# Kernel tuning notes

Hardware: AMD Instinct MI355X
Metric: run time of the kernel (lower is better)

## Reference

```python
import jax, jax.numpy as jnp
import numpy as np

V, E, HL, HH, T_STEPS, N_STEPS = 32000, 768, 1024, 768, 5, 3
B, S = 8, 256
EPS = 1e-5


def _ln(x, g, b):
    m = jnp.mean(x, axis=-1, keepdims=True)
    v = jnp.var(x, axis=-1, keepdims=True)
    return (x - m) * jax.lax.rsqrt(v + EPS) * g + b


def _gru(x, h, Wi, bi, Wh, bh, lni_g, lni_b, lnh_g, lnh_b):
    # Wi: [3, in_dim, H]; gates stacked in order (r, z, n)
    xi = jnp.einsum('bd,kdh->kbh', x, Wi) + bi[:, None, :]
    hi = jnp.einsum('bh,khg->kbg', h, Wh) + bh[:, None, :]
    xi = _ln(xi, lni_g[:, None, :], lni_b[:, None, :])
    hi = _ln(hi, lnh_g[:, None, :], lnh_b[:, None, :])
    r = jax.nn.sigmoid(xi[0] + hi[0])
    z = jax.nn.sigmoid(xi[1] + hi[1])
    n = jnp.tanh(xi[2] + r * hi[2])
    return (1.0 - z) * n + z * h


def setup_inputs() -> dict:
    key = jax.random.key(0)
    ks = jax.random.split(key, 12)
    lin = E + HH  # low-level cell input dim (x concat h_h)

    def xavier(k, shape, fan_in, fan_out):
        lim = float(np.sqrt(6.0 / (fan_in + fan_out)))
        return jax.random.uniform(k, shape, jnp.float32, -lim, lim)

    inp = {
        'input_ids': jax.random.randint(ks[0], (B, S), 0, V),
        'emb': xavier(ks[1], (V, E), V, E),
        'ln_emb_g': jnp.ones((E,), jnp.float32),
        'ln_emb_b': jnp.zeros((E,), jnp.float32),
        'low_Wi': xavier(ks[2], (3, lin, HL), lin, HL),
        'low_bi': jnp.zeros((3, HL), jnp.float32),
        'low_Wh': xavier(ks[3], (3, HL, HL), HL, HL),
        'low_bh': jnp.zeros((3, HL), jnp.float32),
        'low_lni_g': jnp.ones((3, HL), jnp.float32),
        'low_lni_b': jnp.zeros((3, HL), jnp.float32),
        'low_lnh_g': jnp.ones((3, HL), jnp.float32),
        'low_lnh_b': jnp.zeros((3, HL), jnp.float32),
        'high_Wi': xavier(ks[4], (3, HL, HH), HL, HH),
        'high_bi': jnp.zeros((3, HH), jnp.float32),
        'high_Wh': xavier(ks[5], (3, HH, HH), HH, HH),
        'high_bh': jnp.zeros((3, HH), jnp.float32),
        'high_lni_g': jnp.ones((3, HH), jnp.float32),
        'high_lni_b': jnp.zeros((3, HH), jnp.float32),
        'high_lnh_g': jnp.ones((3, HH), jnp.float32),
        'high_lnh_b': jnp.zeros((3, HH), jnp.float32),
        'Wout': xavier(ks[6], (HH, V), HH, V),
        'bout': jnp.zeros((V,), jnp.float32),
    }
    return inp


def reference(input_ids, emb, ln_emb_g, ln_emb_b,
              low_Wi, low_bi, low_Wh, low_bh,
              low_lni_g, low_lni_b, low_lnh_g, low_lnh_b,
              high_Wi, high_bi, high_Wh, high_bh,
              high_lni_g, high_lni_b, high_lnh_g, high_lnh_b,
              Wout, bout):
    b = input_ids.shape[0]
    h_l0 = jnp.zeros((b, HL), jnp.float32)
    h_h0 = jnp.zeros((b, HH), jnp.float32)

    def step(carry, ids_t):
        h_l, h_h = carry
        x = _ln(emb[ids_t], ln_emb_g, ln_emb_b)  # [B, E]
        for _ in range(N_STEPS):
            for _ in range(T_STEPS):
                h_l = _gru(jnp.concatenate([x, h_h], axis=-1), h_l,
                           low_Wi, low_bi, low_Wh, low_bh,
                           low_lni_g, low_lni_b, low_lnh_g, low_lnh_b)
            h_h = _gru(h_l, h_h,
                       high_Wi, high_bi, high_Wh, high_bh,
                       high_lni_g, high_lni_b, high_lnh_g, high_lnh_b)
        logits_t = h_h @ Wout + bout  # [B, V]
        return (h_l, h_h), logits_t

    _, logits = jax.lax.scan(step, (h_l0, h_h0), input_ids.T)  # [S, B, V]
    return jnp.transpose(logits, (1, 0, 2))  # [B, S, V]
```

## Files before the change

### kernel.cpp

```cpp
#include <hip/hip_runtime.h>
#include <hip/hip_bf16.h>


#define NWG 128
#define NTH 256
#define EPSV 1e-5f
#define NROUND 4608

typedef __attribute__((ext_vector_type(4))) float f32x4;
typedef __attribute__((ext_vector_type(8))) short short8;
typedef unsigned long long u64;

struct PArgs {
  const int* ids; const float* emb; const float* lng; const float* lnb;
  const float* lWi; const float* lbi; const float* lWh; const float* lbh;
  const float* llig; const float* llib; const float* llhg; const float* llhb;
  const float* hWi; const float* hbi; const float* hWh; const float* hbh;
  const float* hlig; const float* hlib; const float* hlhg; const float* hlhb;
  int* arr; int* rel; int* cnt; u64* sredG; u64* statsG; float* hlR; float* hhR;
  __hip_bfloat16* hist; float* WiT; float* hWiT; float* hWhT;
};

__device__ __forceinline__ float sigm(float x) { return 1.f / (1.f + __expf(-x)); }
__device__ __forceinline__ float tanh_f(float x) {
  x = fminf(15.f, fmaxf(-15.f, x));
  float e = __expf(2.f * x);
  return (e - 1.f) / (e + 1.f);
}
__device__ __forceinline__ int aldi(const int* p) {
  return __hip_atomic_load(p, __ATOMIC_RELAXED, __HIP_MEMORY_SCOPE_AGENT);
}
__device__ __forceinline__ u64 aldu(const u64* p) {
  return __hip_atomic_load(p, __ATOMIC_RELAXED, __HIP_MEMORY_SCOPE_AGENT);
}
__device__ __forceinline__ void asti(int* p, int v) {
  __hip_atomic_store(p, v, __ATOMIC_RELAXED, __HIP_MEMORY_SCOPE_AGENT);
}
__device__ __forceinline__ u64 pk2(float a, float b) {
  union { u64 u; float f[2]; } c; c.f[0] = a; c.f[1] = b; return c.u;
}
__device__ __forceinline__ void astu(u64* p, u64 v) {
  __hip_atomic_store(p, v, __ATOMIC_RELAXED, __HIP_MEMORY_SCOPE_AGENT);
}
__device__ __forceinline__ void ast(float* p, float v) {
  __hip_atomic_store(p, v, __ATOMIC_RELAXED, __HIP_MEMORY_SCOPE_AGENT);
}
__device__ __forceinline__ void ald4x8(const float* p0, const float* p1,
                                       const float* p2, const float* p3,
                                       const float* p4, const float* p5,
                                       const float* p6, const float* p7,
                                       float4& a, float4& b, float4& c, float4& d,
                                       float4& e, float4& f, float4& g, float4& h) {
  asm volatile(
      "global_load_dwordx4 %0, %8, off sc1\n\t"
      "global_load_dwordx4 %1, %9, off sc1\n\t"
      "global_load_dwordx4 %2, %10, off sc1\n\t"
      "global_load_dwordx4 %3, %11, off sc1\n\t"
      "global_load_dwordx4 %4, %12, off sc1\n\t"
      "global_load_dwordx4 %5, %13, off sc1\n\t"
      "global_load_dwordx4 %6, %14, off sc1\n\t"
      "global_load_dwordx4 %7, %15, off sc1\n\t"
      "s_waitcnt vmcnt(0)"
      : "=&v"(a), "=&v"(b), "=&v"(c), "=&v"(d),
        "=&v"(e), "=&v"(f), "=&v"(g), "=&v"(h)
      : "v"(p0), "v"(p1), "v"(p2), "v"(p3),
        "v"(p4), "v"(p5), "v"(p6), "v"(p7)
      : "memory");
}
__device__ __forceinline__ void ald4x4(const float* p0, const float* p1,
                                       const float* p2, const float* p3,
                                       float4& a, float4& b, float4& c, float4& d) {
  asm volatile(
      "global_load_dwordx4 %0, %4, off sc1\n\t"
      "global_load_dwordx4 %1, %5, off sc1\n\t"
      "global_load_dwordx4 %2, %6, off sc1\n\t"
      "global_load_dwordx4 %3, %7, off sc1\n\t"
      "s_waitcnt vmcnt(0)"
      : "=&v"(a), "=&v"(b), "=&v"(c), "=&v"(d)
      : "v"(p0), "v"(p1), "v"(p2), "v"(p3)
      : "memory");
}
__device__ __forceinline__ void ald4x3(const float* p0, const float* p1,
                                       const float* p2,
                                       float4& a, float4& b, float4& c) {
  asm volatile(
      "global_load_dwordx4 %0, %3, off sc1\n\t"
      "global_load_dwordx4 %1, %4, off sc1\n\t"
      "global_load_dwordx4 %2, %5, off sc1\n\t"
      "s_waitcnt vmcnt(0)"
      : "=&v"(a), "=&v"(b), "=&v"(c)
      : "v"(p0), "v"(p1), "v"(p2)
      : "memory");
}

__global__ void __launch_bounds__(NTH) hrm_recur(PArgs P) {
  __shared__ float WhS[24 * 1024];
  __shared__ float Bb[8 * 1024];
  __shared__ float XW[24 * 8];
  __shared__ float xiNs[24 * 8];
  __shared__ float stg[2 * 24 * 8];
  __shared__ float sred[96];
  __shared__ float xm[8], xrs[8];
  __shared__ float mbuf[96][4];
  __shared__ int idsh[8];
  __shared__ int okf;

  const int tid = threadIdx.x;

  if (blockIdx.x >= NWG) {
    const int pl = blockIdx.x - NWG;
    #pragma unroll 1
    for (int r = 1; r <= NROUND; ++r) {
      if (tid < 64) {
        const u64* ap = (const u64*)(P.arr + pl * 128) + tid;
        int lim = 1 << 22, g1 = 1;
        for (;;) {
          u64 v = aldu(ap);
          int a0 = (int)(unsigned)(v & 0xffffffffull);
          int a1 = (int)(unsigned)(v >> 32);
          if (__all(a0 >= r && a1 >= r)) break;
          if (--lim == 0) { g1 = 0; break; }
          __builtin_amdgcn_s_sleep(1);
        }
        if (tid == 0) okf = g1;
      }
      __syncthreads();
      if (!okf) {
        if (tid < 8) asti(P.rel + pl * 128 + tid * 16, 1 << 30);
        return;
      }
      const int ph = (r - 1) % 6;
      const bool full = (ph == 0 || ph == 5);
      const int lo = pl * 24 + (full ? 0 : 12);
      const int n  = full ? 24 : 12;
      const float invD = (ph == 5) ? (1.f / 768.f) : (1.f / 1024.f);
      const int par = r & 1;
      if (tid < (n >> 1) * 8) {
        int rp = (lo >> 1) + (tid >> 3), q = tid & 7;
        const float* fb = (const float*)(P.statsG + (size_t)par * 128 * 48);
        float4 s; s.x = 0.f; s.y = 0.f; s.z = 0.f; s.w = 0.f;
        #pragma unroll
        for (int blk = 0; blk < 2; ++blk) {
          int w0 = q * 16 + blk * 8;
          float4 t0,t1,t2,t3,t4,t5,t6,t7;
          ald4x8(fb + (size_t)(w0+0)*96 + rp*4, fb + (size_t)(w0+1)*96 + rp*4,
                 fb + (size_t)(w0+2)*96 + rp*4, fb + (size_t)(w0+3)*96 + rp*4,
                 fb + (size_t)(w0+4)*96 + rp*4, fb + (size_t)(w0+5)*96 + rp*4,
                 fb + (size_t)(w0+6)*96 + rp*4, fb + (size_t)(w0+7)*96 + rp*4,
                 t0,t1,t2,t3,t4,t5,t6,t7);
          s.x += t0.x+t1.x+t2.x+t3.x+t4.x+t5.x+t6.x+t7.x;
          s.y += t0.y+t1.y+t2.y+t3.y+t4.y+t5.y+t6.y+t7.y;
          s.z += t0.z+t1.z+t2.z+t3.z+t4.z+t5.z+t6.z+t7.z;
          s.w += t0.w+t1.w+t2.w+t3.w+t4.w+t5.w+t6.w+t7.w;
        }
        mbuf[tid][0] = s.x; mbuf[tid][1] = s.y; mbuf[tid][2] = s.z; mbuf[tid][3] = s.w;
      }
      __syncthreads();
      if (tid < n) {
        int rpl = tid >> 1, comp = tid & 1;
        float s1 = 0.f, s2 = 0.f;
        #pragma unroll
        for (int q = 0; q < 8; ++q) {
          s1 += mbuf[rpl * 8 + q][comp * 2 + 0];
          s2 += mbuf[rpl * 8 + q][comp * 2 + 1];
        }
        float m = s1 * invD;
        float rs = rsqrtf(s2 * invD - m * m + EPSV);
        astu(P.sredG + (size_t)pl * 96 + (size_t)par * 48 + lo + tid, pk2(m, rs));
      }
      asm volatile("s_waitcnt vmcnt(0)" ::: "memory");
      __syncthreads();
      if (tid < 8) asti(P.rel + pl * 128 + tid * 16, r);
    }
    return;
  }

  const int wg = blockIdx.x;
  const int ks = tid & 31, cg = tid >> 5;
  const int lj8 = wg * 8, lj6 = wg * 6;
  const int rep = wg & 3;

  auto arriveA = [&](int pl, int r) {
    asm volatile("s_waitcnt vmcnt(0)" ::: "memory");
    __syncthreads();
    if (tid == 0) asti(P.arr + pl * 128 + wg, r);
  };
  auto pollRel = [&](int pl, int r, bool full) -> bool {
    if (tid == 0) {
      const int* rp = P.rel + pl * 128 + (wg & 7) * 16;
      int lim = 1 << 22, v = 0;
      do {
        v = aldi(rp);
        if (v >= r) break;
        __builtin_amdgcn_s_sleep(1);
      } while (--lim);
      okf = (lim != 0 && v < (1 << 29)) ? 1 : 0;
    }
    __syncthreads();
    if (okf) {
      int lo = pl * 24 + (full ? 0 : 12);
      int n  = full ? 24 : 12;
      if (tid < n) {
        int row = lo + tid;
        union { u64 u; float f[2]; } c;
        c.u = aldu(P.sredG + (size_t)pl * 96 + (size_t)(r & 1) * 48 + row);
        int local = row - pl * 24;
        int set = local / 12, rem = local % 12, g = rem >> 2, bq = rem & 3;
        int b = pl * 4 + bq;
        sred[set * 48 + g * 16 + b * 2] = c.f[0];
        sred[set * 48 + g * 16 + b * 2 + 1] = c.f[1];
      }
      __syncthreads();
    }
    return okf != 0;
  };
  auto waitB = [&](int pl, int target) -> bool {
    if (tid < 64) {
      bool active = tid < 8;
      const int* cp = P.cnt + pl * 256 + (size_t)(active ? tid : 0) * 32;
      int lim = 1 << 22;
      for (;;) {
        int v = active ? aldi(cp) : 0;
        int sum = v;
        sum += __shfl_xor(sum, 1);
        sum += __shfl_xor(sum, 2);
        sum += __shfl_xor(sum, 4);
        int total = __shfl(sum, 0);
        if (total >= target) break;
        if (--lim == 0) break;
        __builtin_amdgcn_s_sleep(2);
      }
      if (tid == 0) okf = (lim != 0) ? 1 : 0;
    }
    __syncthreads();
    return okf != 0;
  };
  auto gate_commit = [&](int pl) {
    asm volatile("s_waitcnt vmcnt(0)" ::: "memory");
    if (tid == 0)
      __hip_atomic_fetch_add(P.cnt + pl * 256 + (size_t)(wg & 7) * 32, 1,
                             __ATOMIC_RELAXED, __HIP_MEMORY_SCOPE_AGENT);
  };

  auto stage_hl = [&](int pl) {
    const float* base = P.hlR + (size_t)rep * 8192 + (size_t)pl * 4096 + tid * 4;
    float4 t0,t1,t2,t3;
    ald4x4(base + 0*1024, base + 1*1024, base + 2*1024, base + 3*1024,
           t0,t1,t2,t3);
    float* db = &Bb[pl * 4096 + tid * 4];
    *(float4*)&db[0*1024] = t0; *(float4*)&db[1*1024] = t1;
    *(float4*)&db[2*1024] = t2; *(float4*)&db[3*1024] = t3;
  };
  auto stage_hh = [&](int pl) {
    const float* base = P.hhR + (size_t)rep * 6144 + (size_t)pl * 3072;
    int bi[3], ki[3];
    #pragma unroll
    for (int i = 0; i < 3; ++i) {
      int c = i * 256 + tid; int bq = c / 192; int k = (c - bq * 192) * 4;
      bi[i] = bq; ki[i] = k;
    }
    float4 t0,t1,t2;
    ald4x3(base + bi[0]*768 + ki[0], base + bi[1]*768 + ki[1],
           base + bi[2]*768 + ki[2], t0,t1,t2);
    *(float4*)&Bb[(pl*4+bi[0])*1024 + ki[0]] = t0;
    *(float4*)&Bb[(pl*4+bi[1])*1024 + ki[1]] = t1;
    *(float4*)&Bb[(pl*4+bi[2])*1024 + ki[2]] = t2;
  };

  auto gemm_lowh = [&](int pl, float (&acc)[3][4]) {
    const int c0 = cg * 3;
    const float* w0p = &WhS[(c0 + 0) * 1024];
    const float* w1p = &WhS[(c0 + 1) * 1024];
    const float* w2p = &WhS[(c0 + 2) * 1024];
    const float* hb = &Bb[pl * 4096];
    #pragma unroll
    for (int i = 0; i < 8; ++i) {
      int k = i * 128 + ks * 4;
      float4 w0 = *(const float4*)&w0p[k];
      float4 w1 = *(const float4*)&w1p[k];
      float4 w2 = *(const float4*)&w2p[k];
      #pragma unroll
      for (int bq = 0; bq < 4; ++bq) {
        float4 h = *(const float4*)&hb[bq * 1024 + k];
        acc[0][bq] += w0.x*h.x + w0.y*h.y + w0.z*h.z + w0.w*h.w;
        acc[1][bq] += w1.x*h.x + w1.y*h.y + w1.z*h.z + w1.w*h.w;
        acc[2][bq] += w2.x*h.x + w2.y*h.y + w2.z*h.z + w2.w*h.w;
      }
    }
  };
  auto gemm_xih = [&](int pl, float (&acc)[3][4]) {
    const float* wp[3];
    #pragma unroll
    for (int cc = 0; cc < 3; ++cc) {
      int c = cg * 3 + cc; int g = c >> 3, jj = c & 7;
      wp[cc] = P.WiT + ((size_t)g * 1024 + lj8 + jj) * 1536 + 768;
    }
    const float* hb = &Bb[pl * 4096];
    #pragma unroll
    for (int i = 0; i < 6; ++i) {
      int k = i * 128 + ks * 4;
      float4 w0 = *(const float4*)&wp[0][k];
      float4 w1 = *(const float4*)&wp[1][k];
      float4 w2 = *(const float4*)&wp[2][k];
      #pragma unroll
      for (int bq = 0; bq < 4; ++bq) {
        float4 h = *(const float4*)&hb[bq * 1024 + k];
        acc[0][bq] += w0.x*h.x + w0.y*h.y + w0.z*h.z + w0.w*h.w;
        acc[1][bq] += w1.x*h.x + w1.y*h.y + w1.z*h.z + w1.w*h.w;
        acc[2][bq] += w2.x*h.x + w2.y*h.y + w2.z*h.z + w2.w*h.w;
      }
    }
  };
  auto gemm_hxi = [&](int pl, float (&acc)[3][4]) {
    if (cg >= 6) return;
    const float* wp[3];
    #pragma unroll
    for (int cc = 0; cc < 3; ++cc) {
      int c = cg * 3 + cc; int g = c / 6, jj = c % 6;
      wp[cc] = P.hWiT + ((size_t)g * 768 + lj6 + jj) * 1024;
    }
    const float* hb = &Bb[pl * 4096];
    #pragma unroll
    for (int i = 0; i < 8; ++i) {
      int k = i * 128 + ks * 4;
      float4 w0 = *(const float4*)&wp[0][k];
      float4 w1 = *(const float4*)&wp[1][k];
      float4 w2 = *(const float4*)&wp[2][k];
      #pragma unroll
      for (int bq = 0; bq < 4; ++bq) {
        float4 h = *(const float4*)&hb[bq * 1024 + k];
        acc[0][bq] += w0.x*h.x + w0.y*h.y + w0.z*h.z + w0.w*h.w;
        acc[1][bq] += w1.x*h.x + w1.y*h.y + w1.z*h.z + w1.w*h.w;
        acc[2][bq] += w2.x*h.x + w2.y*h.y + w2.z*h.z + w2.w*h.w;
      }
    }
  };
  auto gemm_hhh = [&](int pl, float (&acc)[3][4]) {
    if (cg >= 6) return;
    const float* wp[3];
    #pragma unroll
    for (int cc = 0; cc < 3; ++cc) {
      int c = cg * 3 + cc; int g = c / 6, jj = c % 6;
      wp[cc] = P.hWhT + ((size_t)g * 768 + lj6 + jj) * 768;
    }
    const float* hb = &Bb[pl * 4096];
    #pragma unroll
    for (int i = 0; i < 6; ++i) {
      int k = i * 128 + ks * 4;
      float4 w0 = *(const float4*)&wp[0][k];
      float4 w1 = *(const float4*)&wp[1][k];
      float4 w2 = *(const float4*)&wp[2][k];
      #pragma unroll
      for (int bq = 0; bq < 4; ++bq) {
        float4 h = *(const float4*)&hb[bq * 1024 + k];
        acc[0][bq] += w0.x*h.x + w0.y*h.y + w0.z*h.z + w0.w*h.w;
        acc[1][bq] += w1.x*h.x + w1.y*h.y + w1.z*h.z + w1.w*h.w;
        acc[2][bq] += w2.x*h.x + w2.y*h.y + w2.z*h.z + w2.w*h.w;
      }
    }
  };

  auto redstage = [&](int pl, float (&acc)[3][4], int set, const float* bias,
                      int dim, int perg, int jb, bool addXW) {
    #pragma unroll
    for (int cc = 0; cc < 3; ++cc)
      #pragma unroll
      for (int bq = 0; bq < 4; ++bq) {
        float v = acc[cc][bq];
        #pragma unroll
        for (int m = 1; m < 32; m <<= 1) v += __shfl_xor(v, m, 64);
        acc[cc][bq] = v;
      }
    if ((tid & 31) == 0) {
      int cgl = tid >> 5;
      #pragma unroll
      for (int cc = 0; cc < 3; ++cc) {
        int c = cgl * 3 + cc;
        if (c < perg * 3) {
          int g = (perg == 8) ? (c >> 3) : (c / 6);
          int jj = (perg == 8) ? (c & 7) : (c % 6);
          float bs = bias[g * dim + jb + jj];
          #pragma unroll
          for (int bq = 0; bq < 4; ++bq) {
            float v = acc[cc][bq] + bs;
            if (addXW) v += XW[c * 8 + pl * 4 + bq];
            stg[set * 192 + c * 8 + pl * 4 + bq] = v;
          }
        }
      }
    }
  };

  auto stats_put = [&](int pl, int par, int set, int perg) {
    if (tid < 12) {
      int g = tid >> 2, bq = tid & 3;
      float s1 = 0.f, s2 = 0.f;
      for (int jj = 0; jj < perg; ++jj) {
        float v = stg[set * 192 + (g * perg + jj) * 8 + pl * 4 + bq];
        s1 += v; s2 += v * v;
      }
      int row = pl * 24 + set * 12 + g * 4 + bq;
      astu(P.statsG + ((size_t)par * 128 + wg) * 48 + row, pk2(s1, s2));
    }
  };

  auto gate_low = [&](int pl, bool isA) {
    if (tid < 32) {
      int jj = tid & 7, bq = tid >> 3; int b = pl * 4 + bq; int j = lj8 + jj;
      float xin[3], hin[3];
      #pragma unroll
      for (int g = 0; g < 3; ++g) {
        int c = g * 8 + jj;
        if (isA) {
          float m = sred[g * 16 + b * 2], rs = sred[g * 16 + b * 2 + 1];
          float v = (stg[c * 8 + b] - m) * rs * P.llig[g * 1024 + j] + P.llib[g * 1024 + j];
          xiNs[c * 8 + b] = v; xin[g] = v;
        } else {
          xin[g] = xiNs[c * 8 + b];
        }
        float m2 = sred[48 + g * 16 + b * 2], rs2 = sred[48 + g * 16 + b * 2 + 1];
        hin[g] = (stg[192 + c * 8 + b] - m2) * rs2 * P.llhg[g * 1024 + j] + P.llhb[g * 1024 + j];
      }
      float rg = sigm(xin[0] + hin[0]);
      float zg = sigm(xin[1] + hin[1]);
      float ng = tanh_f(xin[2] + rg * hin[2]);
      float hold = Bb[b * 1024 + j];
      float hv = (1.f - zg) * ng + zg * hold;
      #pragma unroll
      for (int rp = 0; rp < 4; ++rp) ast(&P.hlR[rp * 8192 + b * 1024 + j], hv);
    }
  };

  auto gate_high = [&](int pl, int t, int nn) {
    if (tid < 24) {
      int jj = tid % 6, bq = tid / 6; int b = pl * 4 + bq; int j = lj6 + jj;
      float xin[3], hin[3];
      #pragma unroll
      for (int g = 0; g < 3; ++g) {
        int c = g * 6 + jj;
        float m = sred[g * 16 + b * 2], rs = sred[g * 16 + b * 2 + 1];
        xin[g] = (stg[c * 8 + b] - m) * rs * P.hlig[g * 768 + j] + P.hlib[g * 768 + j];
        float m2 = sred[48 + g * 16 + b * 2], rs2 = sred[48 + g * 16 + b * 2 + 1];
        hin[g] = (stg[192 + c * 8 + b] - m2) * rs2 * P.hlhg[g * 768 + j] + P.hlhb[g * 768 + j];
      }
      float rg = sigm(xin[0] + hin[0]);
      float zg = sigm(xin[1] + hin[1]);
      float ng = tanh_f(xin[2] + rg * hin[2]);
      float hold = Bb[b * 1024 + j];
      float hv = (1.f - zg) * ng + zg * hold;
      #pragma unroll
      for (int rp = 0; rp < 4; ++rp) ast(&P.hhR[rp * 6144 + b * 768 + j], hv);
      if (nn == 2) P.hist[((size_t)t * 8 + b) * 768 + j] = __float2bfloat16(hv);
    }
  };

  auto xfun = [&](int tt) {
    int bq = tid >> 5, u = tid & 31;
    if (tid < 8) idsh[tid] = P.ids[tid * 256 + tt];
    int id = P.ids[bq * 256 + tt];
    const float* e = P.emb + (size_t)id * 768;
    float s1 = 0.f, s2 = 0.f;
    #pragma unroll
    for (int q = 0; q < 24; q += 4) {
      float4 v = *(const float4*)&e[u * 24 + q];
      s1 += v.x + v.y + v.z + v.w;
      s2 += v.x*v.x + v.y*v.y + v.z*v.z + v.w*v.w;
    }
    #pragma unroll
    for (int m = 1; m < 32; m <<= 1) { s1 += __shfl_xor(s1, m, 64); s2 += __shfl_xor(s2, m, 64); }
    if (u == 0) { float mm = s1 / 768.f; xm[bq] = mm; xrs[bq] = rsqrtf(s2 / 768.f - mm * mm + EPSV); }
    __syncthreads();
    float acc[3][8] = {};
    const float* wp[3];
    #pragma unroll
    for (int cc = 0; cc < 3; ++cc) {
      int c = cg * 3 + cc; int g = c >> 3, jj = c & 7;
      wp[cc] = P.WiT + ((size_t)g * 1024 + lj8 + jj) * 1536;
    }
    int idv[8];
    #pragma unroll
    for (int bb = 0; bb < 8; ++bb) idv[bb] = idsh[bb];
// ... 57 lines not shown
      float vv[6] = {a.x, a.y, b2v.x, b2v.y, c2v.x, c2v.y};
      for (int jj = 0; jj < 6; ++jj)
        P.hWiT[((size_t)g * 768 + lj6 + jj) * 1024 + k] = vv[jj];
    }
  #pragma unroll 1
  for (int g = 0; g < 3; ++g)
    for (int it = 0; it < 3; ++it) {
      int k = it * 256 + tid;
      const float* src = P.hWh + ((size_t)g * 768 + k) * 768 + lj6;
      float2 a = *(const float2*)src, b2v = *(const float2*)(src + 2), c2v = *(const float2*)(src + 4);
      float vv[6] = {a.x, a.y, b2v.x, b2v.y, c2v.x, c2v.y};
      for (int jj = 0; jj < 6; ++jj)
        P.hWhT[((size_t)g * 768 + lj6 + jj) * 768 + k] = vv[jj];
    }
  #pragma unroll 1
  for (int g = 0; g < 3; ++g)
    for (int it = 0; it < 4; ++it) {
      int k = it * 256 + tid;
      const float* src = P.lWh + ((size_t)g * 1024 + k) * 1024 + lj8;
      float4 v0 = *(const float4*)src; float4 v1 = *(const float4*)(src + 4);
      float vv[8] = {v0.x, v0.y, v0.z, v0.w, v1.x, v1.y, v1.z, v1.w};
      for (int jj = 0; jj < 8; ++jj) WhS[(g * 8 + jj) * 1024 + k] = vv[jj];
    }
  __syncthreads();
  xfun(0);

  int r = 1;
  bool alive = true;
  #pragma unroll 1
  for (int t = 0; t < 256 && alive; ++t) {
    #pragma unroll 1
    for (int nn = 0; nn < 3 && alive; ++nn) {
      {
        #pragma unroll 1
        for (int pl = 0; pl < 2; ++pl) {
          alive = waitB(pl, NWG * (r - 1)); if (!alive) break;
          stage_hh(pl); __syncthreads();
          float aX[3][4] = {};
          gemm_xih(pl, aX);
          redstage(pl, aX, 0, P.lbi, 1024, 8, lj8, true);
          __syncthreads();
          stage_hl(pl); __syncthreads();
          float aH[3][4] = {};
          gemm_lowh(pl, aH);
          redstage(pl, aH, 1, P.lbh, 1024, 8, lj8, false);
          __syncthreads();
          stats_put(pl, r & 1, 0, 8); stats_put(pl, r & 1, 1, 8);
          arriveA(pl, r);
        }
        if (!alive) break;
        #pragma unroll 1
        for (int pl = 0; pl < 2; ++pl) {
          alive = pollRel(pl, r, true); if (!alive) break;
          gate_low(pl, true);
          gate_commit(pl);
        }
        if (!alive) break;
        ++r;
      }
      #pragma unroll 1
      for (int it = 1; it < 5 && alive; ++it) {
        #pragma unroll 1
        for (int pl = 0; pl < 2; ++pl) {
          alive = waitB(pl, NWG * (r - 1)); if (!alive) break;
          stage_hl(pl); __syncthreads();
          float a2[3][4] = {};
          gemm_lowh(pl, a2);
          redstage(pl, a2, 1, P.lbh, 1024, 8, lj8, false);
          __syncthreads();
          stats_put(pl, r & 1, 1, 8);
          arriveA(pl, r);
        }
        if (!alive) break;
        #pragma unroll 1
        for (int pl = 0; pl < 2; ++pl) {
          alive = pollRel(pl, r, false); if (!alive) break;
          gate_low(pl, false);
          gate_commit(pl);
        }
        if (!alive) break;
        ++r;
      }
      if (!alive) break;
      {
        #pragma unroll 1
        for (int pl = 0; pl < 2; ++pl) {
          alive = waitB(pl, NWG * (r - 1)); if (!alive) break;
          stage_hl(pl); __syncthreads();
          float aX[3][4] = {};
          gemm_hxi(pl, aX);
          redstage(pl, aX, 0, P.hbi, 768, 6, lj6, false);
          __syncthreads();
          stage_hh(pl); __syncthreads();
          float aH[3][4] = {};
          gemm_hhh(pl, aH);
          redstage(pl, aH, 1, P.hbh, 768, 6, lj6, false);
          __syncthreads();
          stats_put(pl, r & 1, 0, 6); stats_put(pl, r & 1, 1, 6);
          arriveA(pl, r);
        }
        if (!alive) break;
        #pragma unroll 1
        for (int pl = 0; pl < 2; ++pl) {
          alive = pollRel(pl, r, true); if (!alive) break;
          gate_high(pl, t, nn);
          gate_commit(pl);
        }
        if (!alive) break;
        ++r;
        if (nn == 2 && t < 255) { __syncthreads(); xfun(t + 1); }
      }
    }
  }
}

__global__ void __launch_bounds__(256) wout_t(const float* __restrict__ W,
                                              __hip_bfloat16* __restrict__ WT) {
  __shared__ float T[64][65];
  int n0 = blockIdx.x * 64, k0 = blockIdx.y * 64;
  int tid = threadIdx.x;
  int lane16 = tid & 15, grp = tid >> 4;
  #pragma unroll
  for (int i = 0; i < 4; ++i) {
    int kl = i * 16 + grp; int nl = lane16 * 4;
    float4 v = *(const float4*)&W[(size_t)(k0 + kl) * 32000 + n0 + nl];
    T[kl][nl] = v.x; T[kl][nl + 1] = v.y; T[kl][nl + 2] = v.z; T[kl][nl + 3] = v.w;
  }
  __syncthreads();
  #pragma unroll
  for (int i = 0; i < 4; ++i) {
    int nl = i * 16 + grp; int kl = lane16 * 4;
    union { ushort4 v; __hip_bfloat16 h[4]; } u;
    for (int q = 0; q < 4; ++q) u.h[q] = __float2bfloat16(T[kl + q][nl]);
    *(ushort4*)&WT[(size_t)(n0 + nl) * 768 + k0 + kl] = u.v;
  }
}

// ... 35 lines not shown
      for (int j = 0; j < 4; ++j)
        bfr[j] = *(short8*)&Bs[(wc * 64 + j * 16 + r16) * 64 + kk + khalf];
      #pragma unroll
      for (int i = 0; i < 4; ++i)
        #pragma unroll
        for (int j = 0; j < 4; ++j)
          acc[i][j] = __builtin_amdgcn_mfma_f32_16x16x32_bf16(af[i], bfr[j], acc[i][j], 0, 0, 0);
    }
  }
  #pragma unroll
  for (int i = 0; i < 4; ++i)
    #pragma unroll
    for (int j = 0; j < 4; ++j)
      #pragma unroll
      for (int q = 0; q < 4; ++q) {
        int m = m0 + wr * 64 + i * 16 + ((lane >> 4) * 4 + q);
        int n = n0 + wc * 64 + j * 16 + (lane & 15);
        out[(size_t)(m & 7) * 8192000 + (size_t)(m >> 3) * 32000 + n] =
            acc[i][j][q] + bias[n];
      }
}

extern "C" void kernel_launch(void* const* d_in, const int* in_sizes, int n_in,
                              void* d_out, int out_size, void* d_ws, size_t ws_size,
                              hipStream_t stream) {
  (void)in_sizes; (void)n_in; (void)out_size; (void)ws_size;
  char* wsb = (char*)d_ws;
  size_t off = 0;
  auto take = [&](size_t bytes) -> void* {
    void* p = wsb + off;
    off += (bytes + 1023) & ~(size_t)1023;
    return p;
  };
  int* arr    = (int*)take((size_t)2 * 128 * 4);
  int* rel    = (int*)take((size_t)2 * 128 * 4);
  int* cnt    = (int*)take((size_t)2 * 8 * 32 * 4);
  u64* sredG  = (u64*)take((size_t)2 * 2 * 48 * 8);
  float* hlR  = (float*)take((size_t)4 * 8 * 1024 * 4);
  float* hhR  = (float*)take((size_t)4 * 8 * 768 * 4);
  size_t state_bytes = off;
  u64* statsG = (u64*)take((size_t)2 * 128 * 48 * 8);
  __hip_bfloat16* hist = (__hip_bfloat16*)take((size_t)2048 * 768 * 2);
  float* WiT  = (float*)take((size_t)3 * 1024 * 1536 * 4);
  float* hWiT = (float*)take((size_t)3 * 768 * 1024 * 4);
  float* hWhT = (float*)take((size_t)3 * 768 * 768 * 4);
  __hip_bfloat16* WoutT = (__hip_bfloat16*)take((size_t)32000 * 768 * 2);

  hipMemsetAsync(d_ws, 0, state_bytes, stream);

  wout_t<<<dim3(500, 12), 256, 0, stream>>>((const float*)d_in[20], WoutT);

  PArgs A;
  A.ids = (const int*)d_in[0];   A.emb = (const float*)d_in[1];
  A.lng = (const float*)d_in[2]; A.lnb = (const float*)d_in[3];
  A.lWi = (const float*)d_in[4]; A.lbi = (const float*)d_in[5];
  A.lWh = (const float*)d_in[6]; A.lbh = (const float*)d_in[7];
  A.llig = (const float*)d_in[8];  A.llib = (const float*)d_in[9];
  A.llhg = (const float*)d_in[10]; A.llhb = (const float*)d_in[11];
  A.hWi = (const float*)d_in[12];  A.hbi = (const float*)d_in[13];
  A.hWh = (const float*)d_in[14];  A.hbh = (const float*)d_in[15];
  A.hlig = (const float*)d_in[16]; A.hlib = (const float*)d_in[17];
  A.hlhg = (const float*)d_in[18]; A.hlhb = (const float*)d_in[19];
  A.arr = arr; A.rel = rel; A.cnt = cnt; A.sredG = sredG; A.statsG = statsG;
  A.hlR = hlR; A.hhR = hhR;
  A.hist = hist; A.WiT = WiT; A.hWiT = hWiT; A.hWhT = hWhT;

  hrm_recur<<<NWG + 2, NTH, 0, stream>>>(A);

  logits_gemm<<<dim3(250, 16), 256, 0, stream>>>(hist, WoutT,
                                                 (const float*)d_in[21],
                                                 (float*)d_out);
}
```

Before: 59.90 ms.

## Replace dedicated stats-reducer blocks with atomic accumulation and counter polling

Removes the two extra reducer workgroups that gathered per-WG LayerNorm partial sums and released workers via arrive/release flags. Each worker now atomically adds its partial sums into 8 striped accumulators and bumps a striped counter. Every worker then polls the counter and finalizes the mean and rstd itself, double-buffering and zeroing the accumulators by parity. The aim is to cut one global synchronisation hop per phase, at the cost of float atomic contention and every WG redoing the small finalization.

```diff
diff --git a/kernel.cpp b/kernel.cpp
--- a/kernel.cpp
+++ b/kernel.cpp
@@ -5,7 +5,6 @@
 #define NWG 128
 #define NTH 256
 #define EPSV 1e-5f
-#define NROUND 4608
 
 typedef __attribute__((ext_vector_type(4))) float f32x4;
 typedef __attribute__((ext_vector_type(8))) short short8;
@@ -17,7 +16,7 @@
   const float* llig; const float* llib; const float* llhg; const float* llhb;
   const float* hWi; const float* hbi; const float* hWh; const float* hbh;
   const float* hlig; const float* hlib; const float* hlhg; const float* hlhb;
-  int* arr; int* rel; int* cnt; u64* sredG; u64* statsG; float* hlR; float* hhR;
+  int* cnt; int* scnt; float* statsA; float* hlR; float* hhR;
   __hip_bfloat16* hist; float* WiT; float* hWiT; float* hWhT;
 };
 
@@ -30,42 +29,11 @@
 __device__ __forceinline__ int aldi(const int* p) {
   return __hip_atomic_load(p, __ATOMIC_RELAXED, __HIP_MEMORY_SCOPE_AGENT);
 }
-__device__ __forceinline__ u64 aldu(const u64* p) {
-  return __hip_atomic_load(p, __ATOMIC_RELAXED, __HIP_MEMORY_SCOPE_AGENT);
-}
-__device__ __forceinline__ void asti(int* p, int v) {
-  __hip_atomic_store(p, v, __ATOMIC_RELAXED, __HIP_MEMORY_SCOPE_AGENT);
-}
-__device__ __forceinline__ u64 pk2(float a, float b) {
-  union { u64 u; float f[2]; } c; c.f[0] = a; c.f[1] = b; return c.u;
-}
 __device__ __forceinline__ void astu(u64* p, u64 v) {
   __hip_atomic_store(p, v, __ATOMIC_RELAXED, __HIP_MEMORY_SCOPE_AGENT);
 }
 __device__ __forceinline__ void ast(float* p, float v) {
   __hip_atomic_store(p, v, __ATOMIC_RELAXED, __HIP_MEMORY_SCOPE_AGENT);
-}
-__device__ __forceinline__ void ald4x8(const float* p0, const float* p1,
-                                       const float* p2, const float* p3,
-                                       const float* p4, const float* p5,
-                                       const float* p6, const float* p7,
-                                       float4& a, float4& b, float4& c, float4& d,
-                                       float4& e, float4& f, float4& g, float4& h) {
-  asm volatile(
-      "global_load_dwordx4 %0, %8, off sc1\n\t"
-      "global_load_dwordx4 %1, %9, off sc1\n\t"
-      "global_load_dwordx4 %2, %10, off sc1\n\t"
-      "global_load_dwordx4 %3, %11, off sc1\n\t"
-      "global_load_dwordx4 %4, %12, off sc1\n\t"
-      "global_load_dwordx4 %5, %13, off sc1\n\t"
-      "global_load_dwordx4 %6, %14, off sc1\n\t"
-      "global_load_dwordx4 %7, %15, off sc1\n\t"
-      "s_waitcnt vmcnt(0)"
-      : "=&v"(a), "=&v"(b), "=&v"(c), "=&v"(d),
-        "=&v"(e), "=&v"(f), "=&v"(g), "=&v"(h)
-      : "v"(p0), "v"(p1), "v"(p2), "v"(p3),
-        "v"(p4), "v"(p5), "v"(p6), "v"(p7)
-      : "memory");
 }
 __device__ __forceinline__ void ald4x4(const float* p0, const float* p1,
                                        const float* p2, const float* p3,
@@ -101,119 +69,15 @@
   __shared__ float stg[2 * 24 * 8];
   __shared__ float sred[96];
   __shared__ float xm[8], xrs[8];
-  __shared__ float mbuf[96][4];
   __shared__ int idsh[8];
   __shared__ int okf;
 
   const int tid = threadIdx.x;
-
-  if (blockIdx.x >= NWG) {
-    const int pl = blockIdx.x - NWG;
-    #pragma unroll 1
-    for (int r = 1; r <= NROUND; ++r) {
-      if (tid < 64) {
-        const u64* ap = (const u64*)(P.arr + pl * 128) + tid;
-        int lim = 1 << 22, g1 = 1;
-        for (;;) {
-          u64 v = aldu(ap);
-          int a0 = (int)(unsigned)(v & 0xffffffffull);
-          int a1 = (int)(unsigned)(v >> 32);
-          if (__all(a0 >= r && a1 >= r)) break;
-          if (--lim == 0) { g1 = 0; break; }
-          __builtin_amdgcn_s_sleep(1);
-        }
-        if (tid == 0) okf = g1;
-      }
-      __syncthreads();
-      if (!okf) {
-        if (tid < 8) asti(P.rel + pl * 128 + tid * 16, 1 << 30);
-        return;
-      }
-      const int ph = (r - 1) % 6;
-      const bool full = (ph == 0 || ph == 5);
-      const int lo = pl * 24 + (full ? 0 : 12);
-      const int n  = full ? 24 : 12;
-      const float invD = (ph == 5) ? (1.f / 768.f) : (1.f / 1024.f);
-      const int par = r & 1;
-      if (tid < (n >> 1) * 8) {
-        int rp = (lo >> 1) + (tid >> 3), q = tid & 7;
-        const float* fb = (const float*)(P.statsG + (size_t)par * 128 * 48);
-        float4 s; s.x = 0.f; s.y = 0.f; s.z = 0.f; s.w = 0.f;
-        #pragma unroll
-        for (int blk = 0; blk < 2; ++blk) {
-          int w0 = q * 16 + blk * 8;
-          float4 t0,t1,t2,t3,t4,t5,t6,t7;
-          ald4x8(fb + (size_t)(w0+0)*96 + rp*4, fb + (size_t)(w0+1)*96 + rp*4,
-                 fb + (size_t)(w0+2)*96 + rp*4, fb + (size_t)(w0+3)*96 + rp*4,
-                 fb + (size_t)(w0+4)*96 + rp*4, fb + (size_t)(w0+5)*96 + rp*4,
-                 fb + (size_t)(w0+6)*96 + rp*4, fb + (size_t)(w0+7)*96 + rp*4,
-                 t0,t1,t2,t3,t4,t5,t6,t7);
-          s.x += t0.x+t1.x+t2.x+t3.x+t4.x+t5.x+t6.x+t7.x;
-          s.y += t0.y+t1.y+t2.y+t3.y+t4.y+t5.y+t6.y+t7.y;
-          s.z += t0.z+t1.z+t2.z+t3.z+t4.z+t5.z+t6.z+t7.z;
-          s.w += t0.w+t1.w+t2.w+t3.w+t4.w+t5.w+t6.w+t7.w;
-        }
-        mbuf[tid][0] = s.x; mbuf[tid][1] = s.y; mbuf[tid][2] = s.z; mbuf[tid][3] = s.w;
-      }
-      __syncthreads();
-      if (tid < n) {
-        int rpl = tid >> 1, comp = tid & 1;
-        float s1 = 0.f, s2 = 0.f;
-        #pragma unroll
-        for (int q = 0; q < 8; ++q) {
-          s1 += mbuf[rpl * 8 + q][comp * 2 + 0];
-          s2 += mbuf[rpl * 8 + q][comp * 2 + 1];
-        }
-        float m = s1 * invD;
-        float rs = rsqrtf(s2 * invD - m * m + EPSV);
-        astu(P.sredG + (size_t)pl * 96 + (size_t)par * 48 + lo + tid, pk2(m, rs));
-      }
-      asm volatile("s_waitcnt vmcnt(0)" ::: "memory");
-      __syncthreads();
-      if (tid < 8) asti(P.rel + pl * 128 + tid * 16, r);
-    }
-    return;
-  }
-
   const int wg = blockIdx.x;
   const int ks = tid & 31, cg = tid >> 5;
   const int lj8 = wg * 8, lj6 = wg * 6;
   const int rep = wg & 3;
 
-  auto arriveA = [&](int pl, int r) {
-    asm volatile("s_waitcnt vmcnt(0)" ::: "memory");
-    __syncthreads();
-    if (tid == 0) asti(P.arr + pl * 128 + wg, r);
-  };
-  auto pollRel = [&](int pl, int r, bool full) -> bool {
-    if (tid == 0) {
-      const int* rp = P.rel + pl * 128 + (wg & 7) * 16;
-      int lim = 1 << 22, v = 0;
-      do {
-        v = aldi(rp);
-        if (v >= r) break;
-        __builtin_amdgcn_s_sleep(1);
-      } while (--lim);
-      okf = (lim != 0 && v < (1 << 29)) ? 1 : 0;
-    }
-    __syncthreads();
-    if (okf) {
-      int lo = pl * 24 + (full ? 0 : 12);
-      int n  = full ? 24 : 12;
-      if (tid < n) {
-        int row = lo + tid;
-        union { u64 u; float f[2]; } c;
-        c.u = aldu(P.sredG + (size_t)pl * 96 + (size_t)(r & 1) * 48 + row);
-        int local = row - pl * 24;
-        int set = local / 12, rem = local % 12, g = rem >> 2, bq = rem & 3;
-        int b = pl * 4 + bq;
-        sred[set * 48 + g * 16 + b * 2] = c.f[0];
-        sred[set * 48 + g * 16 + b * 2 + 1] = c.f[1];
-      }
-      __syncthreads();
-    }
-    return okf != 0;
-  };
   auto waitB = [&](int pl, int target) -> bool {
     if (tid < 64) {
       bool active = tid < 8;
@@ -242,14 +106,78 @@
                              __ATOMIC_RELAXED, __HIP_MEMORY_SCOPE_AGENT);
   };
 
+  auto zeroStats = [&](int pl, int pz) {
+    if (wg < 8 && tid < 24)
+      astu((u64*)(P.statsA + (((size_t)(pl * 2 + pz) * 24 + tid) * 16) + wg * 2), 0ull);
+  };
+  auto stats_put = [&](int pl, int par, int set, int perg) {
+    if (tid < 12) {
+      int g = tid >> 2, bq = tid & 3;
+      float s1 = 0.f, s2 = 0.f;
+      for (int jj = 0; jj < perg; ++jj) {
+        float v = stg[set * 192 + (g * perg + jj) * 8 + pl * 4 + bq];
+        s1 += v; s2 += v * v;
+      }
+      int row = set * 12 + g * 4 + bq;
+      float* ap = P.statsA + (((size_t)(pl * 2 + par) * 24 + row) * 16) + (wg & 7) * 2;
+      unsafeAtomicAdd(ap, s1);
+      unsafeAtomicAdd(ap + 1, s2);
+    }
+  };
+  auto statsCommit = [&](int pl) {
+    asm volatile("s_waitcnt vmcnt(0)" ::: "memory");
+    if (tid == 0)
+      __hip_atomic_fetch_add(P.scnt + pl * 256 + (size_t)(wg & 7) * 32, 1,
+                             __ATOMIC_RELAXED, __HIP_MEMORY_SCOPE_AGENT);
+  };
+  auto pollStats = [&](int pl, int r, bool full, float invD) -> bool {
+    if (tid < 64) {
+      bool active = tid < 8;
+      const int* cp = P.scnt + pl * 256 + (size_t)(active ? tid : 0) * 32;
+      int lim = 1 << 22;
+      for (;;) {
+        int v = active ? aldi(cp) : 0;
+        int sum = v;
+        sum += __shfl_xor(sum, 1);
+        sum += __shfl_xor(sum, 2);
+        sum += __shfl_xor(sum, 4);
+        int total = __shfl(sum, 0);
+        if (total >= NWG * r) break;
+        if (--lim == 0) break;
+        __builtin_amdgcn_s_sleep(1);
+      }
+      if (tid == 0) okf = (lim != 0) ? 1 : 0;
+    }
+    __syncthreads();
+    if (!okf) return false;
+    int base_row = full ? 0 : 12;
+    int n = full ? 24 : 12;
+    if (tid < n) {
+      int row = base_row + tid;
+      const float* rp = P.statsA + (((size_t)(pl * 2 + (r & 1)) * 24 + row) * 16);
+      float4 a, b, c, d;
+      ald4x4(rp, rp + 4, rp + 8, rp + 12, a, b, c, d);
+      float s1 = a.x + a.z + b.x + b.z + c.x + c.z + d.x + d.z;
+      float s2 = a.y + a.w + b.y + b.w + c.y + c.w + d.y + d.w;
+      float m = s1 * invD;
+      float rs = rsqrtf(s2 * invD - m * m + EPSV);
+      int set = row / 12, rem = row % 12, g = rem >> 2, bq = rem & 3;
+      int b2 = pl * 4 + bq;
+      sred[set * 48 + g * 16 + b2 * 2] = m;
+      sred[set * 48 + g * 16 + b2 * 2 + 1] = rs;
+    }
+    __syncthreads();
+    return true;
+  };
+
   auto stage_hl = [&](int pl) {
     const float* base = P.hlR + (size_t)rep * 8192 + (size_t)pl * 4096 + tid * 4;
-    float4 t0,t1,t2,t3;
-    ald4x4(base + 0*1024, base + 1*1024, base + 2*1024, base + 3*1024,
-           t0,t1,t2,t3);
+    float4 t0, t1, t2, t3;
+    ald4x4(base + 0 * 1024, base + 1 * 1024, base + 2 * 1024, base + 3 * 1024,
+           t0, t1, t2, t3);
     float* db = &Bb[pl * 4096 + tid * 4];
-    *(float4*)&db[0*1024] = t0; *(float4*)&db[1*1024] = t1;
-    *(float4*)&db[2*1024] = t2; *(float4*)&db[3*1024] = t3;
+    *(float4*)&db[0 * 1024] = t0; *(float4*)&db[1 * 1024] = t1;
+    *(float4*)&db[2 * 1024] = t2; *(float4*)&db[3 * 1024] = t3;
   };
   auto stage_hh = [&](int pl) {
     const float* base = P.hhR + (size_t)rep * 6144 + (size_t)pl * 3072;
@@ -259,12 +187,12 @@
       int c = i * 256 + tid; int bq = c / 192; int k = (c - bq * 192) * 4;
       bi[i] = bq; ki[i] = k;
     }
-    float4 t0,t1,t2;
-    ald4x3(base + bi[0]*768 + ki[0], base + bi[1]*768 + ki[1],
-           base + bi[2]*768 + ki[2], t0,t1,t2);
-    *(float4*)&Bb[(pl*4+bi[0])*1024 + ki[0]] = t0;
-    *(float4*)&Bb[(pl*4+bi[1])*1024 + ki[1]] = t1;
-    *(float4*)&Bb[(pl*4+bi[2])*1024 + ki[2]] = t2;
+    float4 t0, t1, t2;
+    ald4x3(base + bi[0] * 768 + ki[0], base + bi[1] * 768 + ki[1],
+           base + bi[2] * 768 + ki[2], t0, t1, t2);
+    *(float4*)&Bb[(pl * 4 + bi[0]) * 1024 + ki[0]] = t0;
+    *(float4*)&Bb[(pl * 4 + bi[1]) * 1024 + ki[1]] = t1;
+    *(float4*)&Bb[(pl * 4 + bi[2]) * 1024 + ki[2]] = t2;
   };
 
   auto gemm_lowh = [&](int pl, float (&acc)[3][4]) {
@@ -391,19 +319,6 @@
     }
   };
 
-  auto stats_put = [&](int pl, int par, int set, int perg) {
-    if (tid < 12) {
-      int g = tid >> 2, bq = tid & 3;
-      float s1 = 0.f, s2 = 0.f;
-      for (int jj = 0; jj < perg; ++jj) {
-        float v = stg[set * 192 + (g * perg + jj) * 8 + pl * 4 + bq];
-        s1 += v; s2 += v * v;
-      }
-      int row = pl * 24 + set * 12 + g * 4 + bq;
-      astu(P.statsG + ((size_t)par * 128 + wg) * 48 + row, pk2(s1, s2));
-    }
-  };
-
   auto gate_low = [&](int pl, bool isA) {
     if (tid < 32) {
       int jj = tid & 7, bq = tid >> 3; int b = pl * 4 + bq; int j = lj8 + jj;
@@ -573,6 +488,7 @@
         #pragma unroll 1
         for (int pl = 0; pl < 2; ++pl) {
           alive = waitB(pl, NWG * (r - 1)); if (!alive) break;
+          zeroStats(pl, (r + 1) & 1);
           stage_hh(pl); __syncthreads();
           float aX[3][4] = {};
           gemm_xih(pl, aX);
@@ -584,12 +500,12 @@
           redstage(pl, aH, 1, P.lbh, 1024, 8, lj8, false);
           __syncthreads();
           stats_put(pl, r & 1, 0, 8); stats_put(pl, r & 1, 1, 8);
-          arriveA(pl, r);
+          statsCommit(pl);
         }
         if (!alive) break;
         #pragma unroll 1
         for (int pl = 0; pl < 2; ++pl) {
-          alive = pollRel(pl, r, true); if (!alive) break;
+          alive = pollStats(pl, r, true, 1.f / 1024.f); if (!alive) break;
           gate_low(pl, true);
           gate_commit(pl);
         }
@@ -601,18 +517,19 @@
         #pragma unroll 1
         for (int pl = 0; pl < 2; ++pl) {
           alive = waitB(pl, NWG * (r - 1)); if (!alive) break;
+          zeroStats(pl, (r + 1) & 1);
           stage_hl(pl); __syncthreads();
           float a2[3][4] = {};
           gemm_lowh(pl, a2);
           redstage(pl, a2, 1, P.lbh, 1024, 8, lj8, false);
           __syncthreads();
           stats_put(pl, r & 1, 1, 8);
-          arriveA(pl, r);
+          statsCommit(pl);
         }
         if (!alive) break;
         #pragma unroll 1
         for (int pl = 0; pl < 2; ++pl) {
-          alive = pollRel(pl, r, false); if (!alive) break;
+          alive = pollStats(pl, r, false, 1.f / 1024.f); if (!alive) break;
           gate_low(pl, false);
           gate_commit(pl);
         }
@@ -624,6 +541,7 @@
         #pragma unroll 1
         for (int pl = 0; pl < 2; ++pl) {
           alive = waitB(pl, NWG * (r - 1)); if (!alive) break;
+          zeroStats(pl, (r + 1) & 1);
           stage_hl(pl); __syncthreads();
           float aX[3][4] = {};
           gemm_hxi(pl, aX);
@@ -635,12 +553,12 @@
           redstage(pl, aH, 1, P.hbh, 768, 6, lj6, false);
           __syncthreads();
           stats_put(pl, r & 1, 0, 6); stats_put(pl, r & 1, 1, 6);
-          arriveA(pl, r);
+          statsCommit(pl);
         }
         if (!alive) break;
         #pragma unroll 1
         for (int pl = 0; pl < 2; ++pl) {
-          alive = pollRel(pl, r, true); if (!alive) break;
+          alive = pollStats(pl, r, true, 1.f / 768.f); if (!alive) break;
           gate_high(pl, t, nn);
           gate_commit(pl);
         }
@@ -742,18 +660,16 @@
     off += (bytes + 1023) & ~(size_t)1023;
     return p;
   };
-  int* arr    = (int*)take((size_t)2 * 128 * 4);
-  int* rel    = (int*)take((size_t)2 * 128 * 4);
-  int* cnt    = (int*)take((size_t)2 * 8 * 32 * 4);
-  u64* sredG  = (u64*)take((size_t)2 * 2 * 48 * 8);
-  float* hlR  = (float*)take((size_t)4 * 8 * 1024 * 4);
-  float* hhR  = (float*)take((size_t)4 * 8 * 768 * 4);
+  int* cnt      = (int*)take((size_t)2 * 8 * 32 * 4);
+  int* scnt     = (int*)take((size_t)2 * 8 * 32 * 4);
+  float* statsA = (float*)take((size_t)2 * 2 * 24 * 16 * 4);
+  float* hlR    = (float*)take((size_t)4 * 8 * 1024 * 4);
+  float* hhR    = (float*)take((size_t)4 * 8 * 768 * 4);
   size_t state_bytes = off;
-  u64* statsG = (u64*)take((size_t)2 * 128 * 48 * 8);
   __hip_bfloat16* hist = (__hip_bfloat16*)take((size_t)2048 * 768 * 2);
-  float* WiT  = (float*)take((size_t)3 * 1024 * 1536 * 4);
-  float* hWiT = (float*)take((size_t)3 * 768 * 1024 * 4);
-  float* hWhT = (float*)take((size_t)3 * 768 * 768 * 4);
+  float* WiT    = (float*)take((size_t)3 * 1024 * 1536 * 4);
+  float* hWiT   = (float*)take((size_t)3 * 768 * 1024 * 4);
+  float* hWhT   = (float*)take((size_t)3 * 768 * 768 * 4);
   __hip_bfloat16* WoutT = (__hip_bfloat16*)take((size_t)32000 * 768 * 2);
 
   hipMemsetAsync(d_ws, 0, state_bytes, stream);
@@ -771,11 +687,11 @@
   A.hWh = (const float*)d_in[14];  A.hbh = (const float*)d_in[15];
   A.hlig = (const float*)d_in[16]; A.hlib = (const float*)d_in[17];
   A.hlhg = (const float*)d_in[18]; A.hlhb = (const float*)d_in[19];
-  A.arr = arr; A.rel = rel; A.cnt = cnt; A.sredG = sredG; A.statsG = statsG;
+  A.cnt = cnt; A.scnt = scnt; A.statsA = statsA;
   A.hlR = hlR; A.hhR = hhR;
   A.hist = hist; A.WiT = WiT; A.hWiT = hWiT; A.hWhT = hWhT;
 
-  hrm_recur<<<NWG + 2, NTH, 0, stream>>>(A);
+  hrm_recur<<<NWG, NTH, 0, stream>>>(A);
 
   logits_gemm<<<dim3(250, 16), 256, 0, stream>>>(hist, WoutT,
                                                  (const float*)d_in[21],
```

Result: slower. 85.40 ms (+42.6%).

## Wait on both batch halves at once and stage all hidden state per round

Applied to the files above, without the earlier changes.

The two per-half barriers (waitB per pl) become one combined wait that polls both counters together. Both halves of h_l and h_h are then loaded into shared memory in a single batch before the two GEMM passes run. A separate Bh buffer holds h_h, so it no longer overwrites h_l staging, which removes several __syncthreads and serialized global load rounds per step. The cost is about 24KB more LDS and a coarser barrier: the second half can no longer start its compute while the first half's data is still in flight.

```diff
diff --git a/kernel.cpp b/kernel.cpp
--- a/kernel.cpp
+++ b/kernel.cpp
@@ -67,35 +67,28 @@
         "v"(p4), "v"(p5), "v"(p6), "v"(p7)
       : "memory");
 }
-__device__ __forceinline__ void ald4x4(const float* p0, const float* p1,
+__device__ __forceinline__ void ald4x6(const float* p0, const float* p1,
                                        const float* p2, const float* p3,
-                                       float4& a, float4& b, float4& c, float4& d) {
+                                       const float* p4, const float* p5,
+                                       float4& a, float4& b, float4& c,
+                                       float4& d, float4& e, float4& f) {
   asm volatile(
-      "global_load_dwordx4 %0, %4, off sc1\n\t"
-      "global_load_dwordx4 %1, %5, off sc1\n\t"
-      "global_load_dwordx4 %2, %6, off sc1\n\t"
-      "global_load_dwordx4 %3, %7, off sc1\n\t"
+      "global_load_dwordx4 %0, %6, off sc1\n\t"
+      "global_load_dwordx4 %1, %7, off sc1\n\t"
+      "global_load_dwordx4 %2, %8, off sc1\n\t"
+      "global_load_dwordx4 %3, %9, off sc1\n\t"
+      "global_load_dwordx4 %4, %10, off sc1\n\t"
+      "global_load_dwordx4 %5, %11, off sc1\n\t"
       "s_waitcnt vmcnt(0)"
-      : "=&v"(a), "=&v"(b), "=&v"(c), "=&v"(d)
-      : "v"(p0), "v"(p1), "v"(p2), "v"(p3)
-      : "memory");
-}
-__device__ __forceinline__ void ald4x3(const float* p0, const float* p1,
-                                       const float* p2,
-                                       float4& a, float4& b, float4& c) {
-  asm volatile(
-      "global_load_dwordx4 %0, %3, off sc1\n\t"
-      "global_load_dwordx4 %1, %4, off sc1\n\t"
-      "global_load_dwordx4 %2, %5, off sc1\n\t"
-      "s_waitcnt vmcnt(0)"
-      : "=&v"(a), "=&v"(b), "=&v"(c)
-      : "v"(p0), "v"(p1), "v"(p2)
+      : "=&v"(a), "=&v"(b), "=&v"(c), "=&v"(d), "=&v"(e), "=&v"(f)
+      : "v"(p0), "v"(p1), "v"(p2), "v"(p3), "v"(p4), "v"(p5)
       : "memory");
 }
 
 __global__ void __launch_bounds__(NTH) hrm_recur(PArgs P) {
   __shared__ float WhS[24 * 1024];
   __shared__ float Bb[8 * 1024];
+  __shared__ float Bh[8 * 768];
   __shared__ float XW[24 * 8];
   __shared__ float xiNs[24 * 8];
   __shared__ float stg[2 * 24 * 8];
@@ -214,19 +207,20 @@
     }
     return okf != 0;
   };
-  auto waitB = [&](int pl, int target) -> bool {
+  auto waitAB = [&](int target) -> bool {
     if (tid < 64) {
-      bool active = tid < 8;
-      const int* cp = P.cnt + pl * 256 + (size_t)(active ? tid : 0) * 32;
+      bool active = tid < 16;
+      int pl = (tid >> 3) & 1, idx = tid & 7;
+      const int* cp = P.cnt + (active ? (pl * 256 + idx * 32) : 0);
       int lim = 1 << 22;
       for (;;) {
         int v = active ? aldi(cp) : 0;
-        int sum = v;
-        sum += __shfl_xor(sum, 1);
-        sum += __shfl_xor(sum, 2);
-        sum += __shfl_xor(sum, 4);
-        int total = __shfl(sum, 0);
-        if (total >= target) break;
+        v += __shfl_xor(v, 1);
+        v += __shfl_xor(v, 2);
+        v += __shfl_xor(v, 4);
+        int sumA = __shfl(v, 0);
+        int sumB = __shfl(v, 8);
+        if (sumA >= target && sumB >= target) break;
         if (--lim == 0) break;
         __builtin_amdgcn_s_sleep(2);
       }
@@ -242,29 +236,34 @@
                              __ATOMIC_RELAXED, __HIP_MEMORY_SCOPE_AGENT);
   };
 
-  auto stage_hl = [&](int pl) {
-    const float* base = P.hlR + (size_t)rep * 8192 + (size_t)pl * 4096 + tid * 4;
-    float4 t0,t1,t2,t3;
-    ald4x4(base + 0*1024, base + 1*1024, base + 2*1024, base + 3*1024,
-           t0,t1,t2,t3);
-    float* db = &Bb[pl * 4096 + tid * 4];
+  auto stage_all_hl = [&]() {
+    const float* base = P.hlR + (size_t)rep * 8192 + tid * 4;
+    float4 t0,t1,t2,t3,t4,t5,t6,t7;
+    ald4x8(base + 0*1024, base + 1*1024, base + 2*1024, base + 3*1024,
+           base + 4*1024, base + 5*1024, base + 6*1024, base + 7*1024,
+           t0,t1,t2,t3,t4,t5,t6,t7);
+    float* db = &Bb[tid * 4];
     *(float4*)&db[0*1024] = t0; *(float4*)&db[1*1024] = t1;
     *(float4*)&db[2*1024] = t2; *(float4*)&db[3*1024] = t3;
-  };
-  auto stage_hh = [&](int pl) {
-    const float* base = P.hhR + (size_t)rep * 6144 + (size_t)pl * 3072;
-    int bi[3], ki[3];
-    #pragma unroll
-    for (int i = 0; i < 3; ++i) {
+    *(float4*)&db[4*1024] = t4; *(float4*)&db[5*1024] = t5;
+    *(float4*)&db[6*1024] = t6; *(float4*)&db[7*1024] = t7;
+  };
+  auto stage_all_hh = [&]() {
+    const float* base = P.hhR + (size_t)rep * 6144;
+    int bi[6], ki[6];
+    #pragma unroll
+    for (int i = 0; i < 6; ++i) {
       int c = i * 256 + tid; int bq = c / 192; int k = (c - bq * 192) * 4;
       bi[i] = bq; ki[i] = k;
     }
-    float4 t0,t1,t2;
-    ald4x3(base + bi[0]*768 + ki[0], base + bi[1]*768 + ki[1],
-           base + bi[2]*768 + ki[2], t0,t1,t2);
-    *(float4*)&Bb[(pl*4+bi[0])*1024 + ki[0]] = t0;
-    *(float4*)&Bb[(pl*4+bi[1])*1024 + ki[1]] = t1;
-    *(float4*)&Bb[(pl*4+bi[2])*1024 + ki[2]] = t2;
+    float4 t0,t1,t2,t3,t4,t5;
+    ald4x6(base + bi[0]*768 + ki[0], base + bi[1]*768 + ki[1],
+           base + bi[2]*768 + ki[2], base + bi[3]*768 + ki[3],
+           base + bi[4]*768 + ki[4], base + bi[5]*768 + ki[5],
+           t0,t1,t2,t3,t4,t5);
+    *(float4*)&Bh[bi[0]*768 + ki[0]] = t0; *(float4*)&Bh[bi[1]*768 + ki[1]] = t1;
+    *(float4*)&Bh[bi[2]*768 + ki[2]] = t2; *(float4*)&Bh[bi[3]*768 + ki[3]] = t3;
+    *(float4*)&Bh[bi[4]*768 + ki[4]] = t4; *(float4*)&Bh[bi[5]*768 + ki[5]] = t5;
   };
 
   auto gemm_lowh = [&](int pl, float (&acc)[3][4]) {
@@ -295,7 +294,7 @@
       int c = cg * 3 + cc; int g = c >> 3, jj = c & 7;
       wp[cc] = P.WiT + ((size_t)g * 1024 + lj8 + jj) * 1536 + 768;
     }
-    const float* hb = &Bb[pl * 4096];
+    const float* hb = &Bh[pl * 3072];
     #pragma unroll
     for (int i = 0; i < 6; ++i) {
       int k = i * 128 + ks * 4;
@@ -304,7 +303,7 @@
       float4 w2 = *(const float4*)&wp[2][k];
       #pragma unroll
       for (int bq = 0; bq < 4; ++bq) {
-        float4 h = *(const float4*)&hb[bq * 1024 + k];
+        float4 h = *(const float4*)&hb[bq * 768 + k];
         acc[0][bq] += w0.x*h.x + w0.y*h.y + w0.z*h.z + w0.w*h.w;
         acc[1][bq] += w1.x*h.x + w1.y*h.y + w1.z*h.z + w1.w*h.w;
         acc[2][bq] += w2.x*h.x + w2.y*h.y + w2.z*h.z + w2.w*h.w;
@@ -343,7 +342,7 @@
       int c = cg * 3 + cc; int g = c / 6, jj = c % 6;
       wp[cc] = P.hWhT + ((size_t)g * 768 + lj6 + jj) * 768;
     }
-    const float* hb = &Bb[pl * 4096];
+    const float* hb = &Bh[pl * 3072];
     #pragma unroll
     for (int i = 0; i < 6; ++i) {
       int k = i * 128 + ks * 4;
@@ -352,7 +351,7 @@
       float4 w2 = *(const float4*)&wp[2][k];
       #pragma unroll
       for (int bq = 0; bq < 4; ++bq) {
-        float4 h = *(const float4*)&hb[bq * 1024 + k];
+        float4 h = *(const float4*)&hb[bq * 768 + k];
         acc[0][bq] += w0.x*h.x + w0.y*h.y + w0.z*h.z + w0.w*h.w;
         acc[1][bq] += w1.x*h.x + w1.y*h.y + w1.z*h.z + w1.w*h.w;
         acc[2][bq] += w2.x*h.x + w2.y*h.y + w2.z*h.z + w2.w*h.w;
@@ -446,7 +445,7 @@
       float rg = sigm(xin[0] + hin[0]);
       float zg = sigm(xin[1] + hin[1]);
       float ng = tanh_f(xin[2] + rg * hin[2]);
-      float hold = Bb[b * 1024 + j];
+      float hold = Bh[b * 768 + j];
       float hv = (1.f - zg) * ng + zg * hold;
       #pragma unroll
       for (int rp = 0; rp < 4; ++rp) ast(&P.hhR[rp * 6144 + b * 768 + j], hv);
@@ -570,15 +569,14 @@
     #pragma unroll 1
     for (int nn = 0; nn < 3 && alive; ++nn) {
       {
+        alive = waitAB(NWG * (r - 1)); if (!alive) break;
+        stage_all_hh(); stage_all_hl();
+        __syncthreads();
         #pragma unroll 1
         for (int pl = 0; pl < 2; ++pl) {
-          alive = waitB(pl, NWG * (r - 1)); if (!alive) break;
-          stage_hh(pl); __syncthreads();
           float aX[3][4] = {};
           gemm_xih(pl, aX);
           redstage(pl, aX, 0, P.lbi, 1024, 8, lj8, true);
-          __syncthreads();
-          stage_hl(pl); __syncthreads();
           float aH[3][4] = {};
           gemm_lowh(pl, aH);
           redstage(pl, aH, 1, P.lbh, 1024, 8, lj8, false);
@@ -586,7 +584,6 @@
           stats_put(pl, r & 1, 0, 8); stats_put(pl, r & 1, 1, 8);
           arriveA(pl, r);
         }
-        if (!alive) break;
         #pragma unroll 1
         for (int pl = 0; pl < 2; ++pl) {
           alive = pollRel(pl, r, true); if (!alive) break;
@@ -598,10 +595,11 @@
       }
       #pragma unroll 1
       for (int it = 1; it < 5 && alive; ++it) {
+        alive = waitAB(NWG * (r - 1)); if (!alive) break;
+        stage_all_hl();
+        __syncthreads();
         #pragma unroll 1
         for (int pl = 0; pl < 2; ++pl) {
-          alive = waitB(pl, NWG * (r - 1)); if (!alive) break;
-          stage_hl(pl); __syncthreads();
           float a2[3][4] = {};
           gemm_lowh(pl, a2);
           redstage(pl, a2, 1, P.lbh, 1024, 8, lj8, false);
@@ -609,7 +607,6 @@
           stats_put(pl, r & 1, 1, 8);
           arriveA(pl, r);
         }
-        if (!alive) break;
         #pragma unroll 1
         for (int pl = 0; pl < 2; ++pl) {
           alive = pollRel(pl, r, false); if (!alive) break;
@@ -621,15 +618,14 @@
       }
       if (!alive) break;
       {
+        alive = waitAB(NWG * (r - 1)); if (!alive) break;
+        stage_all_hl(); stage_all_hh();
+        __syncthreads();
         #pragma unroll 1
         for (int pl = 0; pl < 2; ++pl) {
-          alive = waitB(pl, NWG * (r - 1)); if (!alive) break;
-          stage_hl(pl); __syncthreads();
           float aX[3][4] = {};
           gemm_hxi(pl, aX);
           redstage(pl, aX, 0, P.hbi, 768, 6, lj6, false);
-          __syncthreads();
-          stage_hh(pl); __syncthreads();
           float aH[3][4] = {};
           gemm_hhh(pl, aH);
           redstage(pl, aH, 1, P.hbh, 768, 6, lj6, false);
@@ -637,7 +633,6 @@
           stats_put(pl, r & 1, 0, 6); stats_put(pl, r & 1, 1, 6);
           arriveA(pl, r);
         }
-        if (!alive) break;
         #pragma unroll 1
         for (int pl = 0; pl < 2; ++pl) {
           alive = pollRel(pl, r, true); if (!alive) break;
```

Result: no change. 60.28 ms, median of 2 (+0.6%).
